# Kernel optimization log

Measured on AMD Instinct MI355X. Metric: run time of the kernel, lower is better.

## Reference

```python
import jax, jax.numpy as jnp
import numpy as np


def _gelu(x):
    # tf.nn.gelu default is exact (erf) gelu
    return jax.nn.gelu(x, approximate=False)


def _reduce_gat(x, W, A):
    # x: [..., n, f]; W: [f, d]; A: [2d, 1]
    wx = x @ W                                   # [..., n, d]
    root = jnp.broadcast_to(wx[..., 0:1, :], wx.shape)  # gather idx 0 + repeat
    cat = jnp.concatenate([wx, root], axis=-1)   # [..., n, 2d]
    z = _gelu(cat @ A)                           # Dense(1, activation=gelu)
    att = jax.nn.softmax(_gelu(z), axis=-2)      # gelu applied twice, then softmax over n
    return _gelu(jnp.sum(wx * att, axis=-2))     # [..., d]


def _layer(x, W, A):
    # W: [H, f, d], A: [H, 2d, 1]; mean over heads
    heads = jax.vmap(lambda w, a: _reduce_gat(x, w, a))(W, A)
    return jnp.mean(heads, axis=0)


def setup_inputs() -> dict:
    key = jax.random.key(0)
    k = jax.random.split(key, 5)
    B, N2, N1, F, D, H = 512, 16, 16, 256, 256, 4
    x = jax.random.normal(k[0], (B, N2, N1, F), dtype=jnp.float32)
    W0 = jax.random.normal(k[1], (H, F, D), dtype=jnp.float32) * 0.05
    A0 = jax.random.normal(k[2], (H, 2 * D, 1), dtype=jnp.float32) * 0.05
    W1 = jax.random.normal(k[3], (H, D, D), dtype=jnp.float32) * 0.05
    A1 = jax.random.normal(k[4], (H, 2 * D, 1), dtype=jnp.float32) * 0.05
    return {"x": x, "W0": W0, "A0": A0, "W1": W1, "A1": A1}


def reference(x, W0, A0, W1, A1):
    x = _layer(x, W0, A0)  # [B, N2, D]
    x = _layer(x, W1, A1)  # [B, D]
    return x
```

## Files before the change

kernel.cpp:

```cpp
#include <hip/hip_runtime.h>
#include <math.h>

typedef _Float16 half_t;
typedef __attribute__((ext_vector_type(8))) _Float16 half8;
typedef __attribute__((ext_vector_type(16))) float floatx16;

__device__ __forceinline__ float gelu_exact(float v) {
    return 0.5f * v * (1.0f + erff(v * 0.7071067811865476f));
}

__device__ __forceinline__ floatx16 zero16() {
    floatx16 z;
#pragma unroll
    for (int i = 0; i < 16; ++i) z[i] = 0.f;
    return z;
}

#define MFMA16(a, b, c) __builtin_amdgcn_mfma_f32_32x32x16_f16((a), (b), (c), 0, 0, 0)

__global__ __launch_bounds__(256) void prep(const float* __restrict__ W0,
                                            const float* __restrict__ A0,
                                            const float* __restrict__ W1,
                                            const float* __restrict__ A1,
                                            half_t* __restrict__ Wsw0, half_t* __restrict__ Wsw1,
                                            half_t* __restrict__ Zah0, half_t* __restrict__ Zal0,
                                            half_t* __restrict__ Zah1, half_t* __restrict__ Zal1) {
    __shared__ float tile[32][257];
    const int t  = threadIdx.x;
    const int kb = blockIdx.x & 7;
    const int h  = (blockIdx.x >> 3) & 3;
    const int tz = blockIdx.x >> 5;
    const float* W = tz ? W1 : W0;
    const float* A = tz ? A1 : A0;
    half_t* Wsw = tz ? Wsw1 : Wsw0;
    half_t* Zh  = tz ? Zah1 : Zah0;
    half_t* Zl  = tz ? Zal1 : Zal0;

    for (int i = 0; i < 32; ++i)
        tile[i][t] = W[(size_t)(h * 256 + kb * 32 + i) * 256 + t];
    __syncthreads();

    const int j = t >> 5, lmn = t & 31;
#pragma unroll
    for (int i0 = 0; i0 < 32; i0 += 8) {
        const int ks = 2 * kb + (i0 >> 4);
        const int q  = (i0 >> 3) & 1;
        half_t hb[8];
#pragma unroll
        for (int ii = 0; ii < 8; ++ii) hb[ii] = (half_t)tile[i0 + ii][t];
        size_t off = ((size_t)(h * 16 + ks) * 8 + j) * 512 + (size_t)(32 * q + lmn) * 8;
        *(half8*)&Wsw[off] = *(half8*)hb;
    }

    if (kb == 0) {
        const float4* Wr = (const float4*)&W[(size_t)(h * 256 + t) * 256];
        const float4* Al = (const float4*)&A[h * 512];
        const float4* Ah = (const float4*)&A[h * 512 + 256];
        float wl = 0.f, wh = 0.f;
        for (int d = 0; d < 64; ++d) {
            float4 wv = Wr[d], a0 = Al[d], a1 = Ah[d];
            wl += wv.x * a0.x + wv.y * a0.y + wv.z * a0.z + wv.w * a0.w;
            wh += wv.x * a1.x + wv.y * a1.y + wv.z * a1.z + wv.w * a1.w;
        }
        half_t hi = (half_t)wl;
        Zh[(2 * h) * 256 + t] = hi;
        Zl[(2 * h) * 256 + t] = (half_t)(wl - (float)hi);
        hi = (half_t)wh;
        Zh[(2 * h + 1) * 256 + t] = hi;
        Zl[(2 * h + 1) * 256 + t] = (half_t)(wh - (float)hi);
        if (h == 0) {
            for (int c = 8; c < 32; ++c) {
                Zh[c * 256 + t] = (half_t)0.f;
                Zl[c * 256 + t] = (half_t)0.f;
            }
        }
    }
}

template <int GROUPS>
__global__ __launch_bounds__(256, 2) void gat_layer(
    const float* __restrict__ x,
    const half_t* __restrict__ Wsw,
    const half_t* __restrict__ Zah, const half_t* __restrict__ Zal,
    float* __restrict__ out) {
    constexpr int ROWS = GROUPS * 16;
    constexpr int MT   = ROWS / 32;

    __shared__ half_t xsh[MT * 16 * 512];
    __shared__ half_t xsl[MT * 16 * 512];
    __shared__ float zlo_s[4][ROWS];
    __shared__ float zhi_s[4][ROWS];
    __shared__ float ge_s[4][ROWS];
    __shared__ float att_s[4][ROWS];

    const int t  = threadIdx.x;
    const int w  = t >> 6;
    const int l  = t & 63;
    const int lm = t & 31;
    const int q  = (t >> 5) & 1;

    {
        const float4* xg = (const float4*)(x + (size_t)blockIdx.x * ROWS * 256);
#pragma unroll
        for (int i = 0; i < ROWS / 8; ++i) {
            int e = t + 256 * i;
            int row = e >> 5, cc = e & 31;
            float4 v0 = xg[row * 64 + 2 * cc];
            float4 v1 = xg[row * 64 + 2 * cc + 1];
            half_t hb[8], lb[8];
            const float* vf = &v0.x;
#pragma unroll
            for (int ii = 0; ii < 8; ++ii) {
                float v = (ii < 4) ? vf[ii] : (&v1.x)[ii - 4];
                half_t hv = (half_t)v;
                hb[ii] = hv;
                lb[ii] = (half_t)(v - (float)hv);
            }
            int m = row >> 5, r31 = row & 31, ks = cc >> 1, kq = cc & 1;
            int base = ((m * 16 + ks) * 64 + 32 * kq + r31) * 8;
            *(half8*)&xsh[base] = *(half8*)hb;
            *(half8*)&xsl[base] = *(half8*)lb;
        }
    }
    __syncthreads();

    if (w == 0) {
        floatx16 zm[MT], zc[MT];
#pragma unroll
        for (int mt = 0; mt < MT; ++mt) { zm[mt] = zero16(); zc[mt] = zero16(); }
#pragma unroll 4
        for (int ks = 0; ks < 16; ++ks) {
            const int ko = lm * 256 + 16 * ks + 8 * q;
            half8 bh = *(const half8*)&Zah[ko];
            half8 bl = *(const half8*)&Zal[ko];
#pragma unroll
            for (int mt = 0; mt < MT; ++mt) {
                half8 a  = *(const half8*)&xsh[((mt * 16 + ks) * 64 + l) * 8];
                half8 al = *(const half8*)&xsl[((mt * 16 + ks) * 64 + l) * 8];
                zm[mt] = MFMA16(a, bh, zm[mt]);
                zc[mt] = MFMA16(al, bh, zc[mt]);
                zc[mt] = MFMA16(a, bl, zc[mt]);
            }
        }
        if (lm < 8) {
            int h = lm >> 1;
            float* dst = (lm & 1) ? &zhi_s[h][0] : &zlo_s[h][0];
#pragma unroll
            for (int mt = 0; mt < MT; ++mt)
#pragma unroll
                for (int r = 0; r < 16; ++r) {
                    int row = 32 * mt + 4 * q + (r & 3) + 8 * (r >> 2);
                    dst[row] = zm[mt][r] + zc[mt][r];
                }
        }
    }
    __syncthreads();

    {
        int h = t >> 6, r = t & 63;
        if (r < ROWS) {
            float z = zlo_s[h][r] + zhi_s[h][r & ~15];
            ge_s[h][r] = gelu_exact(gelu_exact(z));
        }
    }
    __syncthreads();
    {
        int h = t >> 6, r = t & 63;
        if (r < ROWS) {
            int g0 = r & ~15;
            float mx = -1e30f;
#pragma unroll
            for (int i = 0; i < 16; ++i) mx = fmaxf(mx, ge_s[h][g0 + i]);
            float s = 0.f;
#pragma unroll
            for (int i = 0; i < 16; ++i) s += expf(ge_s[h][g0 + i] - mx);
            att_s[h][r] = expf(ge_s[h][r] - mx) / s;
        }
    }
    __syncthreads();

    float outp[2][GROUPS];
#pragma unroll
    for (int nt = 0; nt < 2; ++nt)
#pragma unroll
        for (int g = 0; g < GROUPS; ++g) outp[nt][g] = 0.f;

#pragma unroll 1
    for (int h = 0; h < 4; ++h) {
        float tp[2][GROUPS];
#pragma unroll
        for (int nt = 0; nt < 2; ++nt)
#pragma unroll
            for (int g = 0; g < GROUPS; ++g) tp[nt][g] = 0.f;

        const half_t* Bp = Wsw + ((size_t)(h * 16) * 8 + 2 * w) * 512 + (size_t)l * 8;

#pragma unroll 1
        for (int pass = 0; pass < 2; ++pass) {
            const half_t* Xp = pass ? xsl : xsh;
            floatx16 acc[MT][2];
#pragma unroll
            for (int mt = 0; mt < MT; ++mt) { acc[mt][0] = zero16(); acc[mt][1] = zero16(); }

#pragma unroll
            for (int ks = 0; ks < 16; ++ks) {
                half8 b0 = *(const half8*)(Bp + (size_t)ks * 4096);
                half8 b1 = *(const half8*)(Bp + (size_t)ks * 4096 + 512);
#pragma unroll
                for (int mt = 0; mt < MT; ++mt) {
                    half8 a = *(const half8*)&Xp[((mt * 16 + ks) * 64 + l) * 8];
                    acc[mt][0] = MFMA16(a, b0, acc[mt][0]);
                    acc[mt][1] = MFMA16(a, b1, acc[mt][1]);
                }
            }

#pragma unroll
            for (int mt = 0; mt < MT; ++mt)
#pragma unroll
                for (int k = 0; k < 4; ++k) {
                    float4 a4 = *(const float4*)&att_s[h][32 * mt + 4 * q + 8 * k];
#pragma unroll
                    for (int jj = 0; jj < 4; ++jj) {
                        int r = 4 * k + jj;
                        int row = 32 * mt + 4 * q + 8 * k + jj;
                        int g = row >> 4;
                        float av = (&a4.x)[jj];
                        tp[0][g] = fmaf(acc[mt][0][r], av, tp[0][g]);
                        tp[1][g] = fmaf(acc[mt][1][r], av, tp[1][g]);
                    }
                }
        }

#pragma unroll
        for (int nt = 0; nt < 2; ++nt)
#pragma unroll
            for (int g = 0; g < GROUPS; ++g) {
                float s = tp[nt][g] + __shfl_xor(tp[nt][g], 32, 64);
                outp[nt][g] += gelu_exact(s);
            }
    }

    if (q == 0) {
#pragma unroll
        for (int g = 0; g < GROUPS; ++g) {
            size_t ro = ((size_t)blockIdx.x * GROUPS + g) * 256 + 64 * w;
            out[ro + lm]      = 0.25f * outp[0][g];
            out[ro + 32 + lm] = 0.25f * outp[1][g];
        }
    }
}

extern "C" void kernel_launch(void* const* d_in, const int* in_sizes, int n_in,
                              void* d_out, int out_size, void* d_ws, size_t ws_size,
                              hipStream_t stream) {
    const float* x  = (const float*)d_in[0];
    const float* W0 = (const float*)d_in[1];
    const float* A0 = (const float*)d_in[2];
    const float* W1 = (const float*)d_in[3];
    const float* A1 = (const float*)d_in[4];

    char* ws = (char*)d_ws;
    float*  y1   = (float*)ws;
    half_t* Wsw0 = (half_t*)(ws + 8388608);
    half_t* Wsw1 = (half_t*)(ws + 8912896);
    half_t* Zah0 = (half_t*)(ws + 9437184);
    half_t* Zal0 = (half_t*)(ws + 9453568);
    half_t* Zah1 = (half_t*)(ws + 9469952);
    half_t* Zal1 = (half_t*)(ws + 9486336);

    prep<<<64, 256, 0, stream>>>(W0, A0, W1, A1, Wsw0, Wsw1, Zah0, Zal0, Zah1, Zal1);
    gat_layer<4><<<2048, 256, 0, stream>>>(x, Wsw0, Zah0, Zal0, y1);
    gat_layer<2><<<256, 256, 0, stream>>>(y1, Wsw1, Zah1, Zal1, (float*)d_out);
}
```

Baseline: 346.6 us.

## Swizzle shared-memory x tiles and restructure head loop to fuse hi/lo passes

Adds an XOR swizzle to the shared-memory layout of the split-fp16 x tiles so that the MFMA A-operand reads land in fewer LDS bank conflicts. The main projection loop now iterates over two column halves per head rather than over hi/lo passes: each iteration loads one B fragment and issues MFMAs for both the high and low parts of x, then sums the two accumulators before the attention-weighted reduction. This changes which output columns each wave owns and reorders the global loads of W, and it adds index arithmetic for the swizzle.

```diff
diff --git a/kernel.cpp b/kernel.cpp
--- a/kernel.cpp
+++ b/kernel.cpp
@@ -14,6 +14,10 @@
 #pragma unroll
     for (int i = 0; i < 16; ++i) z[i] = 0.f;
     return z;
+}
+
+__device__ __forceinline__ int sw_ci(int ci) {
+    return ci ^ (((ci >> 5) ^ (ci >> 8)) & 31);
 }
 
 #define MFMA16(a, b, c) __builtin_amdgcn_mfma_f32_32x32x16_f16((a), (b), (c), 0, 0, 0)
@@ -108,18 +112,17 @@
             float4 v0 = xg[row * 64 + 2 * cc];
             float4 v1 = xg[row * 64 + 2 * cc + 1];
             half_t hb[8], lb[8];
-            const float* vf = &v0.x;
 #pragma unroll
             for (int ii = 0; ii < 8; ++ii) {
-                float v = (ii < 4) ? vf[ii] : (&v1.x)[ii - 4];
+                float v = (ii < 4) ? (&v0.x)[ii] : (&v1.x)[ii - 4];
                 half_t hv = (half_t)v;
                 hb[ii] = hv;
                 lb[ii] = (half_t)(v - (float)hv);
             }
             int m = row >> 5, r31 = row & 31, ks = cc >> 1, kq = cc & 1;
-            int base = ((m * 16 + ks) * 64 + 32 * kq + r31) * 8;
-            *(half8*)&xsh[base] = *(half8*)hb;
-            *(half8*)&xsl[base] = *(half8*)lb;
+            int cs = sw_ci((m * 16 + ks) * 64 + 32 * kq + r31);
+            *(half8*)&xsh[cs * 8] = *(half8*)hb;
+            *(half8*)&xsl[cs * 8] = *(half8*)lb;
         }
     }
     __syncthreads();
@@ -135,8 +138,9 @@
             half8 bl = *(const half8*)&Zal[ko];
 #pragma unroll
             for (int mt = 0; mt < MT; ++mt) {
-                half8 a  = *(const half8*)&xsh[((mt * 16 + ks) * 64 + l) * 8];
-                half8 al = *(const half8*)&xsl[((mt * 16 + ks) * 64 + l) * 8];
+                int cs = sw_ci((mt * 16 + ks) * 64 + l);
+                half8 a  = *(const half8*)&xsh[cs * 8];
+                half8 al = *(const half8*)&xsl[cs * 8];
                 zm[mt] = MFMA16(a, bh, zm[mt]);
                 zc[mt] = MFMA16(al, bh, zc[mt]);
                 zc[mt] = MFMA16(a, bl, zc[mt]);
@@ -181,39 +185,37 @@
 
     float outp[2][GROUPS];
 #pragma unroll
-    for (int nt = 0; nt < 2; ++nt)
-#pragma unroll
-        for (int g = 0; g < GROUPS; ++g) outp[nt][g] = 0.f;
+    for (int hf = 0; hf < 2; ++hf)
+#pragma unroll
+        for (int g = 0; g < GROUPS; ++g) outp[hf][g] = 0.f;
 
 #pragma unroll 1
     for (int h = 0; h < 4; ++h) {
-        float tp[2][GROUPS];
-#pragma unroll
-        for (int nt = 0; nt < 2; ++nt)
-#pragma unroll
-            for (int g = 0; g < GROUPS; ++g) tp[nt][g] = 0.f;
-
-        const half_t* Bp = Wsw + ((size_t)(h * 16) * 8 + 2 * w) * 512 + (size_t)l * 8;
-
 #pragma unroll 1
-        for (int pass = 0; pass < 2; ++pass) {
-            const half_t* Xp = pass ? xsl : xsh;
-            floatx16 acc[MT][2];
-#pragma unroll
-            for (int mt = 0; mt < MT; ++mt) { acc[mt][0] = zero16(); acc[mt][1] = zero16(); }
+        for (int hf = 0; hf < 2; ++hf) {
+            const int jcol = w + 4 * hf;
+            const half_t* Bp = Wsw + ((size_t)(h * 16) * 8 + jcol) * 512 + (size_t)l * 8;
+
+            floatx16 ah_acc[MT], al_acc[MT];
+#pragma unroll
+            for (int mt = 0; mt < MT; ++mt) { ah_acc[mt] = zero16(); al_acc[mt] = zero16(); }
 
 #pragma unroll
             for (int ks = 0; ks < 16; ++ks) {
-                half8 b0 = *(const half8*)(Bp + (size_t)ks * 4096);
-                half8 b1 = *(const half8*)(Bp + (size_t)ks * 4096 + 512);
+                half8 b = *(const half8*)(Bp + (size_t)ks * 4096);
 #pragma unroll
                 for (int mt = 0; mt < MT; ++mt) {
-                    half8 a = *(const half8*)&Xp[((mt * 16 + ks) * 64 + l) * 8];
-                    acc[mt][0] = MFMA16(a, b0, acc[mt][0]);
-                    acc[mt][1] = MFMA16(a, b1, acc[mt][1]);
+                    int cs = sw_ci((mt * 16 + ks) * 64 + l);
+                    half8 ah = *(const half8*)&xsh[cs * 8];
+                    half8 al = *(const half8*)&xsl[cs * 8];
+                    ah_acc[mt] = MFMA16(ah, b, ah_acc[mt]);
+                    al_acc[mt] = MFMA16(al, b, al_acc[mt]);
                 }
             }
 
+            float tp[GROUPS];
+#pragma unroll
+            for (int g = 0; g < GROUPS; ++g) tp[g] = 0.f;
 #pragma unroll
             for (int mt = 0; mt < MT; ++mt)
 #pragma unroll
@@ -224,28 +226,23 @@
                         int r = 4 * k + jj;
                         int row = 32 * mt + 4 * q + 8 * k + jj;
                         int g = row >> 4;
-                        float av = (&a4.x)[jj];
-                        tp[0][g] = fmaf(acc[mt][0][r], av, tp[0][g]);
-                        tp[1][g] = fmaf(acc[mt][1][r], av, tp[1][g]);
+                        tp[g] = fmaf(ah_acc[mt][r] + al_acc[mt][r], (&a4.x)[jj], tp[g]);
                     }
                 }
-        }
-
-#pragma unroll
-        for (int nt = 0; nt < 2; ++nt)
 #pragma unroll
             for (int g = 0; g < GROUPS; ++g) {
-                float s = tp[nt][g] + __shfl_xor(tp[nt][g], 32, 64);
-                outp[nt][g] += gelu_exact(s);
-            }
+                float s = tp[g] + __shfl_xor(tp[g], 32, 64);
+                outp[hf][g] += gelu_exact(s);
+            }
+        }
     }
 
     if (q == 0) {
 #pragma unroll
         for (int g = 0; g < GROUPS; ++g) {
-            size_t ro = ((size_t)blockIdx.x * GROUPS + g) * 256 + 64 * w;
-            out[ro + lm]      = 0.25f * outp[0][g];
-            out[ro + 32 + lm] = 0.25f * outp[1][g];
+            size_t ro = ((size_t)blockIdx.x * GROUPS + g) * 256;
+            out[ro + 32 * w + lm]        = 0.25f * outp[0][g];
+            out[ro + 128 + 32 * w + lm]  = 0.25f * outp[1][g];
         }
     }
 }
```

Result: slower. 698.0 us (+101.4%).

## Store fp16 split residual as scaled fp8 and use fp8 MFMA correction pass

Applied to the files above, without the earlier changes.

The low part of the fp16 hi/lo split of x is now scaled by 512 and stored as fp8 e4m3 instead of fp16. The correction GEMM runs on fp8 MFMA against fp8-quantised weights, and the result is rescaled afterwards. This halves the LDS footprint of the residual buffer, allowing occupancy to rise from 2 to 3 blocks per CU, and makes the correction pass cheaper. The cost is reduced accuracy in the compensation term and extra fp8 weight buffers built by the prep kernel.

```diff
diff --git a/kernel.cpp b/kernel.cpp
--- a/kernel.cpp
+++ b/kernel.cpp
@@ -1,10 +1,14 @@
 #include <hip/hip_runtime.h>
+#include <hip/hip_fp8.h>
 #include <math.h>
 
 typedef _Float16 half_t;
 typedef __attribute__((ext_vector_type(8))) _Float16 half8;
 typedef __attribute__((ext_vector_type(16))) float floatx16;
 
+#define LO_SCALE 512.0f
+#define INV_LO   0.001953125f
+
 __device__ __forceinline__ float gelu_exact(float v) {
     return 0.5f * v * (1.0f + erff(v * 0.7071067811865476f));
 }
@@ -16,15 +20,25 @@
     return z;
 }
 
+__device__ __forceinline__ unsigned char to_fp8(float v) {
+    __hip_fp8_e4m3 f(v);
+    return f.__x;
+}
+
 #define MFMA16(a, b, c) __builtin_amdgcn_mfma_f32_32x32x16_f16((a), (b), (c), 0, 0, 0)
+#define MFMA8(a, b, c)  __builtin_amdgcn_mfma_f32_32x32x16_fp8_fp8((a), (b), (c), 0, 0, 0)
 
 __global__ __launch_bounds__(256) void prep(const float* __restrict__ W0,
                                             const float* __restrict__ A0,
                                             const float* __restrict__ W1,
                                             const float* __restrict__ A1,
                                             half_t* __restrict__ Wsw0, half_t* __restrict__ Wsw1,
+                                            unsigned char* __restrict__ Wsw8_0,
+                                            unsigned char* __restrict__ Wsw8_1,
                                             half_t* __restrict__ Zah0, half_t* __restrict__ Zal0,
-                                            half_t* __restrict__ Zah1, half_t* __restrict__ Zal1) {
+                                            unsigned char* __restrict__ Za8_0,
+                                            half_t* __restrict__ Zah1, half_t* __restrict__ Zal1,
+                                            unsigned char* __restrict__ Za8_1) {
     __shared__ float tile[32][257];
     const int t  = threadIdx.x;
     const int kb = blockIdx.x & 7;
@@ -33,8 +47,10 @@
     const float* W = tz ? W1 : W0;
     const float* A = tz ? A1 : A0;
     half_t* Wsw = tz ? Wsw1 : Wsw0;
+    unsigned char* W8 = tz ? Wsw8_1 : Wsw8_0;
     half_t* Zh  = tz ? Zah1 : Zah0;
     half_t* Zl  = tz ? Zal1 : Zal0;
+    unsigned char* Z8 = tz ? Za8_1 : Za8_0;
 
     for (int i = 0; i < 32; ++i)
         tile[i][t] = W[(size_t)(h * 256 + kb * 32 + i) * 256 + t];
@@ -46,10 +62,16 @@
         const int ks = 2 * kb + (i0 >> 4);
         const int q  = (i0 >> 3) & 1;
         half_t hb[8];
-#pragma unroll
-        for (int ii = 0; ii < 8; ++ii) hb[ii] = (half_t)tile[i0 + ii][t];
+        unsigned long long pk = 0ull;
+#pragma unroll
+        for (int ii = 0; ii < 8; ++ii) {
+            float v = tile[i0 + ii][t];
+            hb[ii] = (half_t)v;
+            pk |= ((unsigned long long)to_fp8(v)) << (8 * ii);
+        }
         size_t off = ((size_t)(h * 16 + ks) * 8 + j) * 512 + (size_t)(32 * q + lmn) * 8;
         *(half8*)&Wsw[off] = *(half8*)hb;
+        *(unsigned long long*)&W8[off] = pk;
     }
 
     if (kb == 0) {
@@ -64,30 +86,34 @@
         }
         half_t hi = (half_t)wl;
         Zh[(2 * h) * 256 + t] = hi;
-        Zl[(2 * h) * 256 + t] = (half_t)(wl - (float)hi);
+        Zl[(2 * h) * 256 + t] = (half_t)((wl - (float)hi) * LO_SCALE);
+        Z8[(2 * h) * 256 + t] = to_fp8(wl);
         hi = (half_t)wh;
         Zh[(2 * h + 1) * 256 + t] = hi;
-        Zl[(2 * h + 1) * 256 + t] = (half_t)(wh - (float)hi);
+        Zl[(2 * h + 1) * 256 + t] = (half_t)((wh - (float)hi) * LO_SCALE);
+        Z8[(2 * h + 1) * 256 + t] = to_fp8(wh);
         if (h == 0) {
             for (int c = 8; c < 32; ++c) {
                 Zh[c * 256 + t] = (half_t)0.f;
                 Zl[c * 256 + t] = (half_t)0.f;
+                Z8[c * 256 + t] = 0;
             }
         }
     }
 }
 
 template <int GROUPS>
-__global__ __launch_bounds__(256, 2) void gat_layer(
+__global__ __launch_bounds__(256, 3) void gat_layer(
     const float* __restrict__ x,
-    const half_t* __restrict__ Wsw,
+    const half_t* __restrict__ Wsw, const unsigned char* __restrict__ Wsw8,
     const half_t* __restrict__ Zah, const half_t* __restrict__ Zal,
+    const unsigned char* __restrict__ Za8,
     float* __restrict__ out) {
     constexpr int ROWS = GROUPS * 16;
     constexpr int MT   = ROWS / 32;
 
     __shared__ half_t xsh[MT * 16 * 512];
-    __shared__ half_t xsl[MT * 16 * 512];
+    __shared__ __align__(16) unsigned char xsl8[MT * 16 * 512];
     __shared__ float zlo_s[4][ROWS];
     __shared__ float zhi_s[4][ROWS];
     __shared__ float ge_s[4][ROWS];
@@ -107,39 +133,41 @@
             int row = e >> 5, cc = e & 31;
             float4 v0 = xg[row * 64 + 2 * cc];
             float4 v1 = xg[row * 64 + 2 * cc + 1];
-            half_t hb[8], lb[8];
-            const float* vf = &v0.x;
+            half_t hb[8];
+            unsigned long long pk = 0ull;
 #pragma unroll
             for (int ii = 0; ii < 8; ++ii) {
-                float v = (ii < 4) ? vf[ii] : (&v1.x)[ii - 4];
+                float v = (ii < 4) ? (&v0.x)[ii] : (&v1.x)[ii - 4];
                 half_t hv = (half_t)v;
                 hb[ii] = hv;
-                lb[ii] = (half_t)(v - (float)hv);
+                pk |= ((unsigned long long)to_fp8((v - (float)hv) * LO_SCALE)) << (8 * ii);
             }
             int m = row >> 5, r31 = row & 31, ks = cc >> 1, kq = cc & 1;
-            int base = ((m * 16 + ks) * 64 + 32 * kq + r31) * 8;
-            *(half8*)&xsh[base] = *(half8*)hb;
-            *(half8*)&xsl[base] = *(half8*)lb;
+            int ci = (m * 16 + ks) * 64 + 32 * kq + r31;
+            *(half8*)&xsh[ci * 8] = *(half8*)hb;
+            *(unsigned long long*)&xsl8[ci * 8] = pk;
         }
     }
     __syncthreads();
 
     if (w == 0) {
-        floatx16 zm[MT], zc[MT];
-#pragma unroll
-        for (int mt = 0; mt < MT; ++mt) { zm[mt] = zero16(); zc[mt] = zero16(); }
+        floatx16 zm[MT], zc[MT], z8a[MT];
+#pragma unroll
+        for (int mt = 0; mt < MT; ++mt) { zm[mt] = zero16(); zc[mt] = zero16(); z8a[mt] = zero16(); }
 #pragma unroll 4
         for (int ks = 0; ks < 16; ++ks) {
             const int ko = lm * 256 + 16 * ks + 8 * q;
             half8 bh = *(const half8*)&Zah[ko];
             half8 bl = *(const half8*)&Zal[ko];
+            long  b8 = *(const long*)&Za8[ko];
 #pragma unroll
             for (int mt = 0; mt < MT; ++mt) {
-                half8 a  = *(const half8*)&xsh[((mt * 16 + ks) * 64 + l) * 8];
-                half8 al = *(const half8*)&xsl[((mt * 16 + ks) * 64 + l) * 8];
-                zm[mt] = MFMA16(a, bh, zm[mt]);
-                zc[mt] = MFMA16(al, bh, zc[mt]);
-                zc[mt] = MFMA16(a, bl, zc[mt]);
+                int ci = (mt * 16 + ks) * 64 + l;
+                half8 a  = *(const half8*)&xsh[ci * 8];
+                long  a8 = *(const long*)&xsl8[ci * 8];
+                zm[mt]  = MFMA16(a, bh, zm[mt]);
+                zc[mt]  = MFMA16(a, bl, zc[mt]);
+                z8a[mt] = MFMA8(a8, b8, z8a[mt]);
             }
         }
         if (lm < 8) {
@@ -150,7 +178,7 @@
 #pragma unroll
                 for (int r = 0; r < 16; ++r) {
                     int row = 32 * mt + 4 * q + (r & 3) + 8 * (r >> 2);
-                    dst[row] = zm[mt][r] + zc[mt][r];
+                    dst[row] = zm[mt][r] + (zc[mt][r] + z8a[mt][r]) * INV_LO;
                 }
         }
     }
@@ -193,27 +221,22 @@
 #pragma unroll
             for (int g = 0; g < GROUPS; ++g) tp[nt][g] = 0.f;
 
-        const half_t* Bp = Wsw + ((size_t)(h * 16) * 8 + 2 * w) * 512 + (size_t)l * 8;
-
-#pragma unroll 1
-        for (int pass = 0; pass < 2; ++pass) {
-            const half_t* Xp = pass ? xsl : xsh;
+        {
+            const half_t* Bp = Wsw + ((size_t)(h * 16) * 8 + 2 * w) * 512 + (size_t)l * 8;
             floatx16 acc[MT][2];
 #pragma unroll
             for (int mt = 0; mt < MT; ++mt) { acc[mt][0] = zero16(); acc[mt][1] = zero16(); }
-
 #pragma unroll
             for (int ks = 0; ks < 16; ++ks) {
                 half8 b0 = *(const half8*)(Bp + (size_t)ks * 4096);
                 half8 b1 = *(const half8*)(Bp + (size_t)ks * 4096 + 512);
 #pragma unroll
                 for (int mt = 0; mt < MT; ++mt) {
-                    half8 a = *(const half8*)&Xp[((mt * 16 + ks) * 64 + l) * 8];
+                    half8 a = *(const half8*)&xsh[((mt * 16 + ks) * 64 + l) * 8];
                     acc[mt][0] = MFMA16(a, b0, acc[mt][0]);
                     acc[mt][1] = MFMA16(a, b1, acc[mt][1]);
                 }
             }
-
 #pragma unroll
             for (int mt = 0; mt < MT; ++mt)
 #pragma unroll
@@ -231,6 +254,39 @@
                 }
         }
 
+        {
+            const unsigned char* Bp = Wsw8 + ((size_t)(h * 16) * 8 + 2 * w) * 512 + (size_t)l * 8;
+            floatx16 acc[MT][2];
+#pragma unroll
+            for (int mt = 0; mt < MT; ++mt) { acc[mt][0] = zero16(); acc[mt][1] = zero16(); }
+#pragma unroll
+            for (int ks = 0; ks < 16; ++ks) {
+                long b0 = *(const long*)(Bp + (size_t)ks * 4096);
+                long b1 = *(const long*)(Bp + (size_t)ks * 4096 + 512);
+#pragma unroll
+                for (int mt = 0; mt < MT; ++mt) {
+                    long a = *(const long*)&xsl8[((mt * 16 + ks) * 64 + l) * 8];
+                    acc[mt][0] = MFMA8(a, b0, acc[mt][0]);
+                    acc[mt][1] = MFMA8(a, b1, acc[mt][1]);
+                }
+            }
+#pragma unroll
+            for (int mt = 0; mt < MT; ++mt)
+#pragma unroll
+                for (int k = 0; k < 4; ++k) {
+                    float4 a4 = *(const float4*)&att_s[h][32 * mt + 4 * q + 8 * k];
+#pragma unroll
+                    for (int jj = 0; jj < 4; ++jj) {
+                        int r = 4 * k + jj;
+                        int row = 32 * mt + 4 * q + 8 * k + jj;
+                        int g = row >> 4;
+                        float av = (&a4.x)[jj] * INV_LO;
+                        tp[0][g] = fmaf(acc[mt][0][r], av, tp[0][g]);
+                        tp[1][g] = fmaf(acc[mt][1][r], av, tp[1][g]);
+                    }
+                }
+        }
+
 #pragma unroll
         for (int nt = 0; nt < 2; ++nt)
 #pragma unroll
@@ -260,15 +316,21 @@
     const float* A1 = (const float*)d_in[4];
 
     char* ws = (char*)d_ws;
-    float*  y1   = (float*)ws;
-    half_t* Wsw0 = (half_t*)(ws + 8388608);
-    half_t* Wsw1 = (half_t*)(ws + 8912896);
-    half_t* Zah0 = (half_t*)(ws + 9437184);
-    half_t* Zal0 = (half_t*)(ws + 9453568);
-    half_t* Zah1 = (half_t*)(ws + 9469952);
-    half_t* Zal1 = (half_t*)(ws + 9486336);
-
-    prep<<<64, 256, 0, stream>>>(W0, A0, W1, A1, Wsw0, Wsw1, Zah0, Zal0, Zah1, Zal1);
-    gat_layer<4><<<2048, 256, 0, stream>>>(x, Wsw0, Zah0, Zal0, y1);
-    gat_layer<2><<<256, 256, 0, stream>>>(y1, Wsw1, Zah1, Zal1, (float*)d_out);
-}
+    float*         y1     = (float*)ws;
+    half_t*        Wsw0   = (half_t*)(ws + 8388608);
+    half_t*        Wsw1   = (half_t*)(ws + 8912896);
+    unsigned char* Wsw8_0 = (unsigned char*)(ws + 9437184);
+    unsigned char* Wsw8_1 = (unsigned char*)(ws + 9699328);
+    half_t*        Zah0   = (half_t*)(ws + 9961472);
+    half_t*        Zal0   = (half_t*)(ws + 9977856);
+    half_t*        Zah1   = (half_t*)(ws + 9994240);
+    half_t*        Zal1   = (half_t*)(ws + 10010624);
+    unsigned char* Za8_0  = (unsigned char*)(ws + 10027008);
+    unsigned char* Za8_1  = (unsigned char*)(ws + 10035200);
+
+    prep<<<64, 256, 0, stream>>>(W0, A0, W1, A1, Wsw0, Wsw1, Wsw8_0, Wsw8_1,
+                                 Zah0, Zal0, Za8_0, Zah1, Zal1, Za8_1);
+    gat_layer<4><<<2048, 256, 0, stream>>>(x, Wsw0, Wsw8_0, Zah0, Zal0, Za8_0, y1);
+    gat_layer<2><<<256, 256, 0, stream>>>(y1, Wsw1, Wsw8_1, Zah1, Zal1, Za8_1,
+                                          (float*)d_out);
+}
```

After: 785.9 us. 2.27x slower.
